# Optimization experiments

Measured on AMD Instinct MI355X. Metric: run time of the kernel, lower is better.

## Reference

```python
import jax, jax.numpy as jnp
import numpy as np

B, P, D = 64, 256, 768
S = P + 1            # class token + patches
GRID = 16.0          # sqrt(no_of_patches)
N_IMGS = 10000


def setup_inputs() -> dict:
    key = jax.random.key(0)
    ks = jax.random.split(key, 10)
    sc = 1.0 / np.sqrt(D)
    return {
        "x": jax.random.normal(ks[0], (B, S, D), jnp.float32),
        "img_ids": jax.random.randint(ks[1], (B,), 0, N_IMGS),
        "mask": jnp.ones((B, S), jnp.int32),
        "avgs": 0.1 * jax.random.normal(ks[2], (N_IMGS, 2, P), jnp.float32),
        "std_devs": jnp.ones((N_IMGS, 2, P), jnp.float32),
        "Wq": sc * jax.random.normal(ks[3], (D, D), jnp.float32),
        "bq": jnp.zeros((D,), jnp.float32),
        "Wk": sc * jax.random.normal(ks[4], (D, D), jnp.float32),
        "bk": jnp.zeros((D,), jnp.float32),
        "Wv": sc * jax.random.normal(ks[5], (D, D), jnp.float32),
        "bv": jnp.zeros((D,), jnp.float32),
        "noise_x": jax.random.normal(ks[6], (B, P), jnp.float32),  # torch.normal(0, sigma)
        "noise_y": jax.random.normal(ks[7], (B, P), jnp.float32),
    }


def reference(x, img_ids, mask, avgs, std_devs, Wq, bq, Wk, bk, Wv, bv, noise_x, noise_y):
    # nn.Linear: y = x @ W^T + b
    q = jnp.einsum("bsd,ed->bse", x, Wq) + bq  # (B,S,D)
    k = jnp.einsum("bsd,ed->bse", x, Wk) + bk
    v = jnp.einsum("bsd,ed->bse", x, Wv) + bv

    a = avgs[img_ids]       # (B,2,P)
    sd = std_devs[img_ids]  # (B,2,P)
    half = (GRID - 1.0) / 2.0
    kx = half * (1.0 + jnp.tanh((noise_x + a[:, 0]) * sd[:, 0]))  # (B,P) in (0, GRID-1)
    ky = half * (1.0 + jnp.tanh((noise_y + a[:, 1]) * sd[:, 1]))
    kx1, kx2 = jnp.ceil(kx), jnp.floor(kx)
    ky1, ky2 = jnp.ceil(ky), jnp.floor(ky)

    # corner order matches original: (x1,y1), (x2,y1), (x1,y2), (x2,y2)
    cx = jnp.stack([kx1, kx2, kx1, kx2], axis=1)  # (B,4,P)
    cy = jnp.stack([ky1, ky1, ky2, ky2], axis=1)
    idxs = jax.lax.stop_gradient(GRID * cy + cx).astype(jnp.int32)  # (B,4,P), < P

    sk = jnp.take_along_axis(k[:, None], idxs[..., None], axis=2)  # (B,4,P,D)
    sv = jnp.take_along_axis(v[:, None], idxs[..., None], axis=2)
    cls = jnp.ones((B, 4, 1, D), sk.dtype)
    skf = jnp.concatenate([cls, sk], axis=2)  # (B,4,S,D)
    svf = jnp.concatenate([cls, sv], axis=2)

    # score per query s against its 4 sampled corner keys; softmax over the 4 corners
    scores = jnp.einsum("bnsd,bsd->bsn", skf, q)   # (B,S,4)
    attn = jax.nn.softmax(scores, axis=-1)          # (B,S,4)
    attn_v = attn.transpose(0, 2, 1)[..., None] * svf  # (B,4,S,D)

    # bilinear weights (1-|cx-kx|)*(1-|cy-ky|); class-token weight fixed to 1
    w = (1.0 - jnp.abs(cx - kx[:, None])) * (1.0 - jnp.abs(cy - ky[:, None]))  # (B,4,P)
    wf = jnp.concatenate([jnp.ones((B, 4, 1), w.dtype), w], axis=2)  # (B,4,S)
    out = jnp.einsum("bns,bnsd->bsd", wf, attn_v)  # (B,S,D)
    return out
```

## Files before the change

### kernel.cpp

```cpp
#include <hip/hip_runtime.h>
#include <math.h>


typedef _Float16 f16x8 __attribute__((ext_vector_type(8)));
typedef _Float16 f16x4 __attribute__((ext_vector_type(4)));
typedef float    f32x4 __attribute__((ext_vector_type(4)));

#define MTOT 16448
#define DD   768
#define NC   2304
#define KT   24
#define XCH (129*24*512)
#define WCH (18*24*512)

__global__ __launch_bounds__(256) void prepass(
    const float* __restrict__ x,
    const float* __restrict__ Wq, const float* __restrict__ Wk, const float* __restrict__ Wv,
    _Float16* __restrict__ xp, _Float16* __restrict__ wp)
{
    const int gidx = blockIdx.x * 256 + threadIdx.x;
    const float* src;
    _Float16* dst;
    if (gidx < XCH) {
        const int c = gidx & 511, kk = (gidx >> 9) % KT, t = gidx / (KT * 512);
        const int row = ((c >> 6) << 4) + (c & 15);
        int gm = t * 128 + row; gm = gm < MTOT ? gm : MTOT - 1;
        src = x + (size_t)gm * DD + kk * 32 + ((c >> 4) & 3) * 8;
        dst = xp + (size_t)gidx * 8;
    } else {
        const int g = gidx - XCH;
        const int c = g & 511, kk = (g >> 9) % KT, t = g / (KT * 512);
        const int wrow = t * 128 + ((c >> 6) << 4) + (c & 15);
        const float* W = wrow < 768 ? Wq : (wrow < 1536 ? Wk : Wv);
        const int srow = wrow - (wrow < 768 ? 0 : (wrow < 1536 ? 768 : 1536));
        src = W + (size_t)srow * DD + kk * 32 + ((c >> 4) & 3) * 8;
        dst = wp + (size_t)g * 8;
    }
    const float4 a = *(const float4*)src;
    const float4 b = *(const float4*)(src + 4);
    f16x8 o;
    o[0] = (_Float16)a.x; o[1] = (_Float16)a.y; o[2] = (_Float16)a.z; o[3] = (_Float16)a.w;
    o[4] = (_Float16)b.x; o[5] = (_Float16)b.y; o[6] = (_Float16)b.z; o[7] = (_Float16)b.w;
    *(f16x8*)dst = o;
}

#define GLD(srcp, ldsp) \
    __builtin_amdgcn_global_load_lds( \
        (const __attribute__((address_space(1))) void*)(srcp), \
        (__attribute__((address_space(3))) void*)(ldsp), 16, 0, 0)

__global__ __launch_bounds__(256) void qkv_gemm(
    const _Float16* __restrict__ xp, const _Float16* __restrict__ wp,
    const float* __restrict__ bq, const float* __restrict__ bk, const float* __restrict__ bv,
    _Float16* __restrict__ qkv)
{
    __shared__ __align__(16) _Float16 Ax[2][4096];
    __shared__ __align__(16) _Float16 Bx[2][4096];

    const int bid = blockIdx.x;
    const int xcd = bid & 7, pos = bid >> 3;
    const int q8 = 2322 / 8, r8 = 2322 % 8;
    const int orig = (xcd < r8) ? xcd * (q8 + 1) + pos
                                : r8 * (q8 + 1) + (xcd - r8) * q8 + pos;
    const int tileM = orig / 18, tileN = orig % 18;

    const int tid = threadIdx.x, lane = tid & 63, wid = tid >> 6;
    const int wm = wid >> 1, wn = wid & 1;
    const int r16 = lane & 15, kq = lane >> 4;

    const _Float16* Asrc = xp + (size_t)tileM * KT * 4096;
    const _Float16* Bsrc = wp + (size_t)tileN * KT * 4096;

    const f32x4 zero = {0.f, 0.f, 0.f, 0.f};
    f32x4 acc[4][4];
    #pragma unroll
    for (int i = 0; i < 4; ++i)
        #pragma unroll
        for (int j = 0; j < 4; ++j) acc[i][j] = zero;

    #pragma unroll
    for (int g = 0; g < 2; ++g) {
        const int c0 = g * 256 + wid * 64;
        GLD(Asrc + (size_t)(c0 + lane) * 8, &Ax[0][c0 * 8]);
        GLD(Bsrc + (size_t)(c0 + lane) * 8, &Bx[0][c0 * 8]);
    }
    asm volatile("s_waitcnt vmcnt(0)" ::: "memory");
    __builtin_amdgcn_s_barrier();
    __builtin_amdgcn_sched_barrier(0);

    for (int t = 0; t < KT; ++t) {
        const int cur = t & 1;
        if (t + 1 < KT) {
            const size_t off = (size_t)(t + 1) * 512;
            #pragma unroll
            for (int g = 0; g < 2; ++g) {
                const int c0 = g * 256 + wid * 64;
                GLD(Asrc + (off + c0 + lane) * 8, &Ax[cur ^ 1][c0 * 8]);
                GLD(Bsrc + (off + c0 + lane) * 8, &Bx[cur ^ 1][c0 * 8]);
            }
        }
        __builtin_amdgcn_sched_barrier(0);

        f16x8 a[4], b[4];
        #pragma unroll
        for (int i = 0; i < 4; ++i)
            a[i] = *(const f16x8*)(&Ax[cur][((wm * 4 + i) * 64 + lane) * 8]);
        #pragma unroll
        for (int j = 0; j < 4; ++j)
            b[j] = *(const f16x8*)(&Bx[cur][((wn * 4 + j) * 64 + lane) * 8]);

        __builtin_amdgcn_s_setprio(1);
        #pragma unroll
        for (int i = 0; i < 4; ++i)
            #pragma unroll
            for (int j = 0; j < 4; ++j)
                acc[i][j] = __builtin_amdgcn_mfma_f32_16x16x32_f16(a[i], b[j], acc[i][j], 0, 0, 0);
        __builtin_amdgcn_s_setprio(0);
        __builtin_amdgcn_sched_barrier(0);

        asm volatile("s_waitcnt vmcnt(0)" ::: "memory");
        __builtin_amdgcn_sched_barrier(0);
        __builtin_amdgcn_s_barrier();
        __builtin_amdgcn_sched_barrier(0);
    }

    const int sec = tileN / 6;
    const float* bias = sec == 0 ? bq : (sec == 1 ? bk : bv);
    const int bcol0 = (tileN % 6) * 128 + wn * 64;
    #pragma unroll
    for (int i = 0; i < 4; ++i) {
        const int row0 = tileM * 128 + wm * 64 + i * 16 + kq * 4;
        #pragma unroll
        for (int j = 0; j < 4; ++j) {
            const int col = tileN * 128 + wn * 64 + j * 16 + r16;
            const float bb = bias[bcol0 + j * 16 + r16];
            #pragma unroll
            for (int tt = 0; tt < 4; ++tt) {
                const int row = row0 + tt;
                if (row < MTOT)
                    qkv[(size_t)row * NC + col] = (_Float16)(acc[i][j][tt] + bb);
            }
        }
    }
}

__global__ __launch_bounds__(256) void attn_gather(
    const _Float16* __restrict__ qkv,
    const int*   __restrict__ ids,
    const float* __restrict__ avgs,
    const float* __restrict__ stds,
    const float* __restrict__ nx,
    const float* __restrict__ ny,
    float* __restrict__ out)
{
    const int tid  = threadIdx.x;
    const int lane = tid & 63;
    const int bid = blockIdx.x;
    const int swz = (bid & 7) * 514 + (bid >> 3);
    const int gid = swz * 4 + (tid >> 6);
    const int b = gid / 257, s = gid % 257;
    float* orow = out + (size_t)gid * DD;

    if (s == 0) {
        const float4 one = make_float4(1.f, 1.f, 1.f, 1.f);
        #pragma unroll
        for (int j = 0; j < 3; ++j)
            *(float4*)(orow + 4 * lane + 256 * j) = one;
        return;
    }
    const int p   = s - 1;
    const int img = ids[b];
    const size_t ab = (size_t)img * 512 + p;
    const float a0 = avgs[ab], a1 = avgs[ab + 256];
    const float s0 = stds[ab], s1 = stds[ab + 256];
    const float kx = 7.5f * (1.f + tanhf((nx[b * 256 + p] + a0) * s0));
    const float ky = 7.5f * (1.f + tanhf((ny[b * 256 + p] + a1) * s1));
    const float kx1 = ceilf(kx), kx2 = floorf(kx);
    const float ky1 = ceilf(ky), ky2 = floorf(ky);
    const float cx[4] = {kx1, kx2, kx1, kx2};
    const float cy[4] = {ky1, ky1, ky2, ky2};
    int   idx[4];
    float w[4];
    #pragma unroll
    for (int n = 0; n < 4; ++n) {
        idx[n] = (int)(16.f * cy[n] + cx[n]);
        w[n]   = (1.f - fabsf(cx[n] - kx)) * (1.f - fabsf(cy[n] - ky));
    }

    const _Float16* qrow = qkv + (size_t)gid * NC;
    float qf[12];
    #pragma unroll
    for (int j = 0; j < 3; ++j) {
        const f16x4 v = *(const f16x4*)(qrow + lane * 4 + j * 256);
        qf[4 * j + 0] = (float)v[0]; qf[4 * j + 1] = (float)v[1];
        qf[4 * j + 2] = (float)v[2]; qf[4 * j + 3] = (float)v[3];
    }

    float sc[4];
    #pragma unroll
    for (int n = 0; n < 4; ++n) {
        const _Float16* krow = qkv + (size_t)(b * 257 + idx[n]) * NC + 768;
        float a = 0.f;
        #pragma unroll
        for (int j = 0; j < 3; ++j) {
            const f16x4 kv = *(const f16x4*)(krow + lane * 4 + j * 256);
            a += qf[4 * j + 0] * (float)kv[0] + qf[4 * j + 1] * (float)kv[1]
               + qf[4 * j + 2] * (float)kv[2] + qf[4 * j + 3] * (float)kv[3];
        }
        sc[n] = a;
    }
    #pragma unroll
    for (int n = 0; n < 4; ++n)
        for (int off = 32; off > 0; off >>= 1)
            sc[n] += __shfl_xor(sc[n], off);

    const float mx = fmaxf(fmaxf(sc[0], sc[1]), fmaxf(sc[2], sc[3]));
    const float e0 = expf(sc[0] - mx), e1 = expf(sc[1] - mx),
                e2 = expf(sc[2] - mx), e3 = expf(sc[3] - mx);
    const float inv = 1.f / (e0 + e1 + e2 + e3);
    const float coef[4] = {e0 * inv * w[0], e1 * inv * w[1], e2 * inv * w[2], e3 * inv * w[3]};

    const _Float16* vr0 = qkv + (size_t)(b * 257 + idx[0]) * NC + 1536;
    const _Float16* vr1 = qkv + (size_t)(b * 257 + idx[1]) * NC + 1536;
    const _Float16* vr2 = qkv + (size_t)(b * 257 + idx[2]) * NC + 1536;
    const _Float16* vr3 = qkv + (size_t)(b * 257 + idx[3]) * NC + 1536;
    #pragma unroll
    for (int j = 0; j < 3; ++j) {
        const int d = lane * 4 + j * 256;
        const f16x4 v0 = *(const f16x4*)(vr0 + d);
        const f16x4 v1 = *(const f16x4*)(vr1 + d);
        const f16x4 v2 = *(const f16x4*)(vr2 + d);
        const f16x4 v3 = *(const f16x4*)(vr3 + d);
        float4 o;
        o.x = coef[0] * (float)v0[0] + coef[1] * (float)v1[0] + coef[2] * (float)v2[0] + coef[3] * (float)v3[0];
        o.y = coef[0] * (float)v0[1] + coef[1] * (float)v1[1] + coef[2] * (float)v2[1] + coef[3] * (float)v3[1];
        o.z = coef[0] * (float)v0[2] + coef[1] * (float)v1[2] + coef[2] * (float)v2[2] + coef[3] * (float)v3[2];
        o.w = coef[0] * (float)v0[3] + coef[1] * (float)v1[3] + coef[2] * (float)v2[3] + coef[3] * (float)v3[3];
        *(float4*)(orow + d) = o;
    }
}

extern "C" void kernel_launch(void* const* d_in, const int* in_sizes, int n_in,
                              void* d_out, int out_size, void* d_ws, size_t ws_size,
                              hipStream_t stream) {
    const float* x    = (const float*)d_in[0];
    const int*   ids  = (const int*)  d_in[1];
    const float* avgs = (const float*)d_in[3];
    const float* stds = (const float*)d_in[4];
    const float* Wq   = (const float*)d_in[5];
    const float* bq   = (const float*)d_in[6];
    const float* Wk   = (const float*)d_in[7];
    const float* bk   = (const float*)d_in[8];
    const float* Wv   = (const float*)d_in[9];
    const float* bv   = (const float*)d_in[10];
    const float* nx   = (const float*)d_in[11];
    const float* ny   = (const float*)d_in[12];
    float* out = (float*)d_out;

    char* ws = (char*)d_ws;
    _Float16* qkv = (_Float16*)ws;
    _Float16* xp  = (_Float16*)(ws + 75792384);
    _Float16* wp  = (_Float16*)(ws + 75792384 + 25362432);

    prepass<<<(XCH + WCH) / 256, 256, 0, stream>>>(x, Wq, Wk, Wv, xp, wp);
    qkv_gemm<<<2322, 256, 0, stream>>>(xp, wp, bq, bk, bv, qkv);
    attn_gather<<<4112, 256, 0, stream>>>(qkv, ids, avgs, stds, nx, ny, out);
}
```

Before: 135.2 us.

## Swap MFMA operands for vectorized f16x4 stores, drop LDS double buffering

Swaps the MFMA operand roles so weights feed the A side and activations the B side. Each lane's four accumulator values then lie along contiguous output columns, which allows an 8-byte f16x4 store with a float4 bias load instead of scalar 2-byte stores. The change also removes the double-buffered LDS pipeline, setprio and sched barriers, and instead reloads a single buffer each K step between two __syncthreads. Global-to-LDS load latency is therefore no longer overlapped with MFMA work, in exchange for halving LDS use and simpler code.

```diff
diff --git a/kernel.cpp b/kernel.cpp
--- a/kernel.cpp
+++ b/kernel.cpp
@@ -54,22 +54,22 @@
     const float* __restrict__ bq, const float* __restrict__ bk, const float* __restrict__ bv,
     _Float16* __restrict__ qkv)
 {
-    __shared__ __align__(16) _Float16 Ax[2][4096];
-    __shared__ __align__(16) _Float16 Bx[2][4096];
+    __shared__ __align__(16) _Float16 Wl[4096];
+    __shared__ __align__(16) _Float16 Xl[4096];
 
     const int bid = blockIdx.x;
     const int xcd = bid & 7, pos = bid >> 3;
     const int q8 = 2322 / 8, r8 = 2322 % 8;
     const int orig = (xcd < r8) ? xcd * (q8 + 1) + pos
                                 : r8 * (q8 + 1) + (xcd - r8) * q8 + pos;
-    const int tileM = orig / 18, tileN = orig % 18;
+    const int xtile = orig / 18, wtile = orig % 18;
 
     const int tid = threadIdx.x, lane = tid & 63, wid = tid >> 6;
-    const int wm = wid >> 1, wn = wid & 1;
+    const int wa = wid >> 1, wb = wid & 1;
     const int r16 = lane & 15, kq = lane >> 4;
 
-    const _Float16* Asrc = xp + (size_t)tileM * KT * 4096;
-    const _Float16* Bsrc = wp + (size_t)tileN * KT * 4096;
+    const _Float16* Xsrc = xp + (size_t)xtile * KT * 4096;
+    const _Float16* Wsrc = wp + (size_t)wtile * KT * 4096;
 
     const f32x4 zero = {0.f, 0.f, 0.f, 0.f};
     f32x4 acc[4][4];
@@ -78,67 +78,47 @@
         #pragma unroll
         for (int j = 0; j < 4; ++j) acc[i][j] = zero;
 
-    #pragma unroll
-    for (int g = 0; g < 2; ++g) {
-        const int c0 = g * 256 + wid * 64;
-        GLD(Asrc + (size_t)(c0 + lane) * 8, &Ax[0][c0 * 8]);
-        GLD(Bsrc + (size_t)(c0 + lane) * 8, &Bx[0][c0 * 8]);
-    }
-    asm volatile("s_waitcnt vmcnt(0)" ::: "memory");
-    __builtin_amdgcn_s_barrier();
-    __builtin_amdgcn_sched_barrier(0);
-
-    for (int t = 0; t < KT; ++t) {
-        const int cur = t & 1;
-        if (t + 1 < KT) {
-            const size_t off = (size_t)(t + 1) * 512;
-            #pragma unroll
-            for (int g = 0; g < 2; ++g) {
-                const int c0 = g * 256 + wid * 64;
-                GLD(Asrc + (off + c0 + lane) * 8, &Ax[cur ^ 1][c0 * 8]);
-                GLD(Bsrc + (off + c0 + lane) * 8, &Bx[cur ^ 1][c0 * 8]);
-            }
+    for (int kk = 0; kk < KT; ++kk) {
+        __syncthreads();
+        #pragma unroll
+        for (int g = 0; g < 2; ++g) {
+            const int c0 = g * 256 + wid * 64;
+            GLD(Wsrc + ((size_t)kk * 512 + c0 + lane) * 8, &Wl[c0 * 8]);
+            GLD(Xsrc + ((size_t)kk * 512 + c0 + lane) * 8, &Xl[c0 * 8]);
         }
-        __builtin_amdgcn_sched_barrier(0);
+        __syncthreads();
 
         f16x8 a[4], b[4];
         #pragma unroll
         for (int i = 0; i < 4; ++i)
-            a[i] = *(const f16x8*)(&Ax[cur][((wm * 4 + i) * 64 + lane) * 8]);
+            a[i] = *(const f16x8*)(&Wl[((wa * 4 + i) * 64 + lane) * 8]);
         #pragma unroll
         for (int j = 0; j < 4; ++j)
-            b[j] = *(const f16x8*)(&Bx[cur][((wn * 4 + j) * 64 + lane) * 8]);
-
-        __builtin_amdgcn_s_setprio(1);
+            b[j] = *(const f16x8*)(&Xl[((wb * 4 + j) * 64 + lane) * 8]);
         #pragma unroll
         for (int i = 0; i < 4; ++i)
             #pragma unroll
             for (int j = 0; j < 4; ++j)
                 acc[i][j] = __builtin_amdgcn_mfma_f32_16x16x32_f16(a[i], b[j], acc[i][j], 0, 0, 0);
-        __builtin_amdgcn_s_setprio(0);
-        __builtin_amdgcn_sched_barrier(0);
-
-        asm volatile("s_waitcnt vmcnt(0)" ::: "memory");
-        __builtin_amdgcn_sched_barrier(0);
-        __builtin_amdgcn_s_barrier();
-        __builtin_amdgcn_sched_barrier(0);
-    }
-
-    const int sec = tileN / 6;
+    }
+
+    const int sec = wtile / 6;
     const float* bias = sec == 0 ? bq : (sec == 1 ? bk : bv);
-    const int bcol0 = (tileN % 6) * 128 + wn * 64;
     #pragma unroll
     for (int i = 0; i < 4; ++i) {
-        const int row0 = tileM * 128 + wm * 64 + i * 16 + kq * 4;
+        const int bcol0 = (wtile % 6) * 128 + wa * 64 + i * 16 + kq * 4;
+        const int colg0 = wtile * 128 + wa * 64 + i * 16 + kq * 4;
+        const float4 bb = *(const float4*)(bias + bcol0);
         #pragma unroll
         for (int j = 0; j < 4; ++j) {
-            const int col = tileN * 128 + wn * 64 + j * 16 + r16;
-            const float bb = bias[bcol0 + j * 16 + r16];
-            #pragma unroll
-            for (int tt = 0; tt < 4; ++tt) {
-                const int row = row0 + tt;
-                if (row < MTOT)
-                    qkv[(size_t)row * NC + col] = (_Float16)(acc[i][j][tt] + bb);
+            const int row = xtile * 128 + wb * 64 + j * 16 + r16;
+            if (row < MTOT) {
+                f16x4 o;
+                o[0] = (_Float16)(acc[i][j][0] + bb.x);
+                o[1] = (_Float16)(acc[i][j][1] + bb.y);
+                o[2] = (_Float16)(acc[i][j][2] + bb.z);
+                o[3] = (_Float16)(acc[i][j][3] + bb.w);
+                *(f16x4*)(qkv + (size_t)row * NC + colg0) = o;
             }
         }
     }
```

Measured after the change: 133.4 us. About the same (-1.3%).
